# Kernel tuning notes

Hardware: AMD Instinct MI355X
Metric: run time of the kernel (lower is better)

## Reference

```python
import jax, jax.numpy as jnp
from jax import lax
import numpy as np

B_, C_, H_, W_ = 4, 512, 128, 128   # batch, channels, height, width
HEADS, K, PAD = 8, 3, 1


def setup_inputs() -> dict:
    key = jax.random.key(0)
    ks = jax.random.split(key, 12)
    s = 0.1
    return {
        "output": jax.random.normal(ks[0], (B_, C_, H_, W_), jnp.float32),
        "attn": jax.random.uniform(ks[1], (B_ * W_, HEADS, H_, H_), dtype=jnp.float32),
        "Wv": jax.random.normal(ks[2], (C_, C_), jnp.float32) * 0.02,   # value_conv 1x1
        "bv": jnp.zeros((C_,), jnp.float32),
        "W1": jax.random.normal(ks[3], (K, HEADS, 1, K), jnp.float32) * s,  # conv1 (1,k)
        "b1": jax.random.normal(ks[4], (K,), jnp.float32) * s,
        "W2": jax.random.normal(ks[5], (K, 1, 3, 3), jnp.float32) * s,      # depthwise 3x3
        "b2": jax.random.normal(ks[6], (K,), jnp.float32) * s,
        "Wl": jax.random.normal(ks[7], (K, 1), jnp.float32) * s,            # Linear(1,k)
        "bl": jax.random.normal(ks[8], (K,), jnp.float32) * s,
        "Wo": jax.random.normal(ks[9], (C_, C_), jnp.float32) * 0.02,   # out_conv 1x1
        "bo": jnp.zeros((C_,), jnp.float32),
    }


def _forward(output, attn, Wv, bv, W1, b1, W2, b2, Wl, bl, Wo, bo):
    b, c, h, w = output.shape
    B, heads, p, _ = attn.shape        # B = b*w, p = h (attn_type='height')
    d = c // heads
    k = W1.shape[0]

    # value_conv: 1x1 conv == channel GEMM
    value = jnp.einsum('bchw,oc->bohw', output, Wv) + bv[None, :, None, None]
    # [b,c,h,w] -> [b*w, heads, h, d]
    v = value.transpose(0, 3, 2, 1).reshape(B, p, heads, d).transpose(0, 2, 1, 3)

    # --- Adaptive_kernel: per-position kernel A[b,i,j,m] and per-head gate V[b,n,m] ---
    a = lax.conv_general_dilated(attn, W1, (1, 1), ((0, 0), (PAD, PAD)))
    a = jax.nn.relu(a + b1[None, :, None, None])
    a = lax.conv_general_dilated(a, W2, (1, 1), ((1, 1), (1, 1)), feature_group_count=k)
    a = jax.nn.relu(a + b2[None, :, None, None])
    A = a.transpose(0, 2, 3, 1)                      # [B,p,p,k]
    vm = v.mean(axis=(2, 3))                         # AdaptiveAvgPool2d(1): [B,heads]
    V = vm[..., None] * Wl[:, 0] + bl                # Linear(1,k): [B,heads,k]

    # --- adaptive_conv: involution along width with zero padding ---
    ap = jnp.pad(attn, ((0, 0), (0, 0), (0, 0), (PAD, PAD)))
    attn_new = jnp.zeros_like(attn)
    for m in range(k):  # fixed small kernel width; avoids [B,n,p,p,k] materialization
        attn_new = attn_new + ap[..., m:m + p] * A[:, None, :, :, m] * V[:, :, None, None, m]

    # attn @ value and fold back to [b,c,h,w]
    out = jnp.einsum('bnij,bnjd->bnid', attn_new, v)
    out = out.reshape(b, w, heads, h, d).transpose(0, 2, 4, 3, 1).reshape(b, c, h, w)
    out = jnp.einsum('bchw,oc->bohw', out, Wo) + bo[None, :, None, None]
    return out, attn_new


def reference(output, attn, Wv, bv, W1, b1, W2, b2, Wl, bl, Wo, bo):
    return _forward(output, attn, Wv, bv, W1, b1, W2, b2, Wl, bl, Wo, bo)
```

## Files before the change

kernel.cpp:

```cpp
#include <hip/hip_runtime.h>
#include <hip/hip_bf16.h>

#define BATCH 4
#define C 512
#define H 128
#define W 128
#define HW (H*W)
#define CHW (C*HW)
#define NH 8
#define D 64
#define P 128
#define BB (BATCH*W)
#define OUT0_SIZE ((size_t)BATCH*C*H*W)

__global__ __launch_bounds__(256) void k_gemm_value(
    const float* __restrict__ X, const float* __restrict__ Wv,
    const float* __restrict__ bv, float* __restrict__ out)
{
    const int row = blockIdx.x;
    const int b = row >> 7, h = row & 127;
    const int o0 = blockIdx.y * 128;
    const float* xbase = X + (size_t)b*CHW + (size_t)h*W;
    __shared__ float sA[16][132];
    __shared__ float sB[16][132];
    const int tid = threadIdx.x;
    const int tx = tid & 15, ty = tid >> 4;
    float acc[8][8] = {};
    for (int c0 = 0; c0 < C; c0 += 16) {
        #pragma unroll
        for (int it = 0; it < 8; it++) {
            int f = tid + it*256;
            int m = f >> 4, cc = f & 15;
            sA[cc][m] = Wv[(size_t)(o0+m)*C + c0 + cc];
        }
        #pragma unroll
        for (int it = 0; it < 8; it++) {
            int f = tid + it*256;
            int cc = f >> 7, w = f & 127;
            sB[cc][w] = xbase[(size_t)(c0+cc)*HW + w];
        }
        __syncthreads();
        #pragma unroll
        for (int cc = 0; cc < 16; cc++) {
            float a[8], br[8];
            #pragma unroll
            for (int m = 0; m < 8; m++) a[m] = sA[cc][ty*8+m];
            #pragma unroll
            for (int n = 0; n < 8; n++) br[n] = sB[cc][tx*8+n];
            #pragma unroll
            for (int m = 0; m < 8; m++)
                #pragma unroll
                for (int n = 0; n < 8; n++) acc[m][n] += a[m]*br[n];
        }
        __syncthreads();
    }
    #pragma unroll
    for (int m = 0; m < 8; m++) {
        int o = o0 + ty*8 + m;
        float bias = bv[o];
        float* dst = out + (size_t)b*CHW + (size_t)o*HW + (size_t)h*W + tx*8;
        #pragma unroll
        for (int n = 0; n < 8; n++) dst[n] = acc[m][n] + bias;
    }
}

__global__ __launch_bounds__(256) void k_transpose_v(
    const float* __restrict__ val, float* __restrict__ v)
{
    int g = blockIdx.x;
    int i = g & 127, n = (g >> 7) & 7, b = g >> 10;
    __shared__ float s[64][129];
    int tid = threadIdx.x;
    const float* src = val + (size_t)b*CHW + (size_t)(n*64)*HW + (size_t)i*W;
    #pragma unroll
    for (int it = 0; it < 32; it++) {
        int f = tid + it*256;
        int dd = f >> 7, w = f & 127;
        s[dd][w] = src[(size_t)dd*HW + w];
    }
    __syncthreads();
    float* dst = v + (size_t)n*8192 + (size_t)i*64;
    #pragma unroll
    for (int it = 0; it < 32; it++) {
        int f = tid + it*256;
        int w = f >> 6, dd = f & 63;
        dst[(size_t)(b*W + w)*65536 + dd] = s[dd][w];
    }
}

__global__ __launch_bounds__(256) void k_vm(
    const float* __restrict__ v, float* __restrict__ vm)
{
    int g = blockIdx.x;
    const float4* src = (const float4*)(v + (size_t)g*8192);
    int tid = threadIdx.x;
    float sum = 0.f;
    #pragma unroll
    for (int it = 0; it < 8; it++) {
        float4 x = src[tid + it*256];
        sum += x.x + x.y + x.z + x.w;
    }
    #pragma unroll
    for (int off = 32; off; off >>= 1) sum += __shfl_down(sum, off, 64);
    __shared__ float partial[4];
    if ((tid & 63) == 0) partial[tid >> 6] = sum;
    __syncthreads();
    if (tid == 0) vm[g] = (partial[0]+partial[1]+partial[2]+partial[3]) * (1.0f/8192.0f);
}

__global__ __launch_bounds__(256) void k_conv(
    const float* __restrict__ attn, const float* __restrict__ W1,
    const float* __restrict__ b1, const float* __restrict__ W2,
    const float* __restrict__ b2, float* __restrict__ A)
{
    int blk = blockIdx.x;
    int strip = blk & 7, b = blk >> 3;
    int i0 = strip * 16;
    __shared__ float a1s[3][18][128];
    __shared__ float w1s[72], w2s[27], b1s[3], b2s[3];
    int tid = threadIdx.x;
    if (tid < 72) w1s[tid] = W1[tid];
    else if (tid < 99) w2s[tid-72] = W2[tid-72];
    else if (tid < 102) b1s[tid-99] = b1[tid-99];
    else if (tid < 105) b2s[tid-102] = b2[tid-102];
    __syncthreads();
    const float* abase = attn + (size_t)b*NH*HW;
    for (int it = 0; it < 27; it++) {
        int f = tid + it*256;
        int j = f & 127;
        int r = (f >> 7) % 18;
        int kk = f / 2304;
        int i = i0 - 1 + r;
        float vres = 0.f;
        if (i >= 0 && i < P) {
            float s = b1s[kk];
            #pragma unroll
            for (int n = 0; n < 8; n++) {
                const float* ar = abase + (size_t)n*HW + (size_t)i*W;
                float x0 = (j > 0)   ? ar[j-1] : 0.f;
                float x1 = ar[j];
                float x2 = (j < 127) ? ar[j+1] : 0.f;
                s += x0*w1s[kk*24+n*3+0] + x1*w1s[kk*24+n*3+1] + x2*w1s[kk*24+n*3+2];
            }
            vres = fmaxf(s, 0.f);
        }
        a1s[kk][r][j] = vres;
    }
    __syncthreads();
    for (int it = 0; it < 24; it++) {
        int f = tid + it*256;
        int j = f & 127;
        int lr = (f >> 7) & 15;
        int kk = f >> 11;
        float s = b2s[kk];
        #pragma unroll
        for (int u = 0; u < 3; u++) {
            #pragma unroll
            for (int t = 0; t < 3; t++) {
                int jj = j + t - 1;
                float x = (jj >= 0 && jj < 128) ? a1s[kk][lr+u][jj] : 0.f;
                s += x * w2s[kk*9+u*3+t];
            }
        }
        A[(((size_t)b*3 + kk)*P + (i0+lr))*P + j] = fmaxf(s, 0.f);
    }
}

__global__ __launch_bounds__(256) void k_attn_new(
    const float* __restrict__ attn, const float* __restrict__ A,
    const float* __restrict__ vm, const float* __restrict__ Wl,
    const float* __restrict__ bl, float* __restrict__ anew)
{
    int blk = blockIdx.x;
    int i = blk & 127, bw = blk >> 7;
    __shared__ float As[3][128];
    __shared__ float rows[8][130];
    __shared__ float Vs[8][3];
    int tid = threadIdx.x;
    for (int f = tid; f < 384; f += 256) {
        int m = f >> 7, j = f & 127;
        As[m][j] = A[(((size_t)bw*3 + m)*P + i)*P + j];
    }
    if (tid < 24) {
        int n = tid / 3, m = tid % 3;
        Vs[n][m] = vm[bw*8 + n] * Wl[m] + bl[m];
    }
    const float* ab = attn + (size_t)bw*NH*HW + (size_t)i*W;
    #pragma unroll
    for (int f0 = 0; f0 < 1024; f0 += 256) {
        int f = tid + f0;
        int n = f >> 7, j = f & 127;
        rows[n][j+1] = ab[(size_t)n*HW + j];
    }
    if (tid < 8) { rows[tid][0] = 0.f; rows[tid][129] = 0.f; }
    __syncthreads();
    int n = tid >> 5, jj = tid & 31;
    float v0 = Vs[n][0], v1 = Vs[n][1], v2 = Vs[n][2];
    float* dst = anew + ((size_t)bw*NH + n)*HW + (size_t)i*W;
    #pragma unroll
    for (int q = 0; q < 4; q++) {
        int j = jj + q*32;
        float r = rows[n][j]*As[0][j]*v0 + rows[n][j+1]*As[1][j]*v1 + rows[n][j+2]*As[2][j]*v2;
        dst[j] = r;
    }
}

__global__ __launch_bounds__(256) void k_gemm_av(
    const float* __restrict__ anew, const float* __restrict__ v,
    float* __restrict__ op)
{
    int g = blockIdx.x;
    const float* Abase = anew + (size_t)g*HW;
    const float* Bbase = v + (size_t)g*8192;
    float* obase = op + (size_t)g*8192;
    __shared__ float sAT[16][132];
    __shared__ float sB[16][68];
    int tid = threadIdx.x;
    int tx = tid & 15, ty = tid >> 4;
    float acc[8][4] = {};
    for (int j0 = 0; j0 < 128; j0 += 16) {
        #pragma unroll
        for (int it = 0; it < 8; it++) {
            int f = tid + it*256;
            int i = f >> 4, jc = f & 15;
            sAT[jc][i] = Abase[(size_t)i*128 + j0 + jc];
        }
        #pragma unroll
        for (int it = 0; it < 4; it++) {
            int f = tid + it*256;
            int jc = f >> 6, dd = f & 63;
            sB[jc][dd] = Bbase[(size_t)(j0+jc)*64 + dd];
        }
        __syncthreads();
        #pragma unroll
        for (int jc = 0; jc < 16; jc++) {
            float a[8], br[4];
            #pragma unroll
            for (int m = 0; m < 8; m++) a[m] = sAT[jc][ty*8+m];
            #pragma unroll
            for (int n2 = 0; n2 < 4; n2++) br[n2] = sB[jc][tx*4+n2];
            #pragma unroll
            for (int m = 0; m < 8; m++)
                #pragma unroll
                for (int n2 = 0; n2 < 4; n2++) acc[m][n2] += a[m]*br[n2];
        }
        __syncthreads();
    }
    #pragma unroll
    for (int m = 0; m < 8; m++) {
        float* dst = obase + (size_t)(ty*8+m)*64 + tx*4;
        dst[0]=acc[m][0]; dst[1]=acc[m][1]; dst[2]=acc[m][2]; dst[3]=acc[m][3];
    }
}

__global__ __launch_bounds__(256) void k_gemm_out(
    const float* __restrict__ op, const float* __restrict__ Wo,
    const float* __restrict__ bo, float* __restrict__ out)
{
    int row = blockIdx.x;
    int b = row >> 7, i = row & 127;
    int o0 = blockIdx.y * 128;
    __shared__ float sW[32][132];
    __shared__ float sX[32][132];
    int tid = threadIdx.x;
    int tx = tid & 15, ty = tid >> 4;
    float acc[8][8] = {};
    const float* opbase = op + (size_t)(b*W)*65536 + (size_t)i*64;
    for (int chunk = 0; chunk < 16; chunk++) {
        int c0 = chunk*32;
        int n = c0 >> 6, ddb = c0 & 63;
        #pragma unroll
        for (int it = 0; it < 16; it++) {
            int f = tid + it*256;
            int m = f >> 5, cc = f & 31;
            sW[cc][m] = Wo[(size_t)(o0+m)*C + c0 + cc];
        }
        #pragma unroll
        for (int it = 0; it < 16; it++) {
            int f = tid + it*256;
            int w = f >> 5, cc = f & 31;
            sX[cc][w] = opbase[(size_t)w*65536 + (size_t)n*8192 + ddb + cc];
        }
        __syncthreads();
        #pragma unroll
        for (int cc = 0; cc < 32; cc++) {
            float a[8], br[8];
            #pragma unroll
            for (int m = 0; m < 8; m++) a[m] = sW[cc][ty*8+m];
            #pragma unroll
            for (int nn = 0; nn < 8; nn++) br[nn] = sX[cc][tx*8+nn];
            #pragma unroll
            for (int m = 0; m < 8; m++)
                #pragma unroll
                for (int nn = 0; nn < 8; nn++) acc[m][nn] += a[m]*br[nn];
        }
        __syncthreads();
    }
    #pragma unroll
    for (int m = 0; m < 8; m++) {
        int o = o0 + ty*8 + m;
        float bias = bo[o];
        float* dst = out + (size_t)b*CHW + (size_t)o*HW + (size_t)i*W + tx*8;
        #pragma unroll
        for (int n = 0; n < 8; n++) dst[n] = acc[m][n] + bias;
    }
}

extern "C" void kernel_launch(void* const* d_in, const int* in_sizes, int n_in,
                              void* d_out, int out_size, void* d_ws, size_t ws_size,
                              hipStream_t stream)
{
    const float* X    = (const float*)d_in[0];
    const float* attn = (const float*)d_in[1];
    const float* Wv   = (const float*)d_in[2];
    const float* bv   = (const float*)d_in[3];
    const float* W1   = (const float*)d_in[4];
    const float* b1   = (const float*)d_in[5];
    const float* W2   = (const float*)d_in[6];
    const float* b2   = (const float*)d_in[7];
    const float* Wl   = (const float*)d_in[8];
    const float* bl   = (const float*)d_in[9];
    const float* Wo   = (const float*)d_in[10];
    const float* bo   = (const float*)d_in[11];

    float* out  = (float*)d_out;
    float* anew = (float*)d_out + OUT0_SIZE;

    float* A = out;

    float* ws = (float*)d_ws;
    float* value   = ws;
    float* v       = ws + 33554432;
    float* vm      = ws + 67108864;
    float* out_pre = value;

    k_gemm_value<<<dim3(BATCH*H, C/128), 256, 0, stream>>>(X, Wv, bv, value);
    k_transpose_v<<<BATCH*NH*P, 256, 0, stream>>>(value, v);
    k_vm<<<BB*NH, 256, 0, stream>>>(v, vm);
    k_conv<<<BB*(P/16), 256, 0, stream>>>(attn, W1, b1, W2, b2, A);
    k_attn_new<<<BB*P, 256, 0, stream>>>(attn, A, vm, Wl, bl, anew);
    k_gemm_av<<<BB*NH, 256, 0, stream>>>(anew, v, out_pre);
    k_gemm_out<<<dim3(BATCH*P, C/128), 256, 0, stream>>>(out_pre, Wo, bo, out);
}
```

Before: 1.967 ms.

## Use split-bf16 MFMA for value and output 1x1 conv GEMMs

Replaces the two FP32 SIMT channel GEMMs with MFMA bf16 kernels that emulate fp32 through hi/lo bf16 splitting (three MFMAs per tile). Input X is transposed into channel-contiguous hi/lo buffers, and the value GEMM now writes directly into the per-head v layout, which removes the separate transpose kernel. The attention GEMM emits hi/lo bf16 outputs for the final GEMM. The aim is to move the dominant GEMM FLOPs onto matrix cores, at the cost of extra conversion passes, operands loaded straight from global memory without LDS staging, and slightly reduced precision.

```diff
diff --git a/kernel.cpp b/kernel.cpp
--- a/kernel.cpp
+++ b/kernel.cpp
@@ -1,5 +1,9 @@
 #include <hip/hip_runtime.h>
 #include <hip/hip_bf16.h>
+
+typedef __attribute__((ext_vector_type(8))) short bf16x8;
+typedef __attribute__((ext_vector_type(4))) float f32x4;
+typedef __attribute__((ext_vector_type(4))) unsigned short u16x4;
 
 #define BATCH 4
 #define C 512
@@ -13,78 +17,112 @@
 #define BB (BATCH*W)
 #define OUT0_SIZE ((size_t)BATCH*C*H*W)
 
-__global__ __launch_bounds__(256) void k_gemm_value(
-    const float* __restrict__ X, const float* __restrict__ Wv,
-    const float* __restrict__ bv, float* __restrict__ out)
-{
-    const int row = blockIdx.x;
-    const int b = row >> 7, h = row & 127;
-    const int o0 = blockIdx.y * 128;
-    const float* xbase = X + (size_t)b*CHW + (size_t)h*W;
-    __shared__ float sA[16][132];
-    __shared__ float sB[16][132];
-    const int tid = threadIdx.x;
-    const int tx = tid & 15, ty = tid >> 4;
-    float acc[8][8] = {};
-    for (int c0 = 0; c0 < C; c0 += 16) {
-        #pragma unroll
-        for (int it = 0; it < 8; it++) {
-            int f = tid + it*256;
-            int m = f >> 4, cc = f & 15;
-            sA[cc][m] = Wv[(size_t)(o0+m)*C + c0 + cc];
-        }
-        #pragma unroll
-        for (int it = 0; it < 8; it++) {
-            int f = tid + it*256;
-            int cc = f >> 7, w = f & 127;
-            sB[cc][w] = xbase[(size_t)(c0+cc)*HW + w];
-        }
-        __syncthreads();
-        #pragma unroll
-        for (int cc = 0; cc < 16; cc++) {
-            float a[8], br[8];
-            #pragma unroll
-            for (int m = 0; m < 8; m++) a[m] = sA[cc][ty*8+m];
-            #pragma unroll
-            for (int n = 0; n < 8; n++) br[n] = sB[cc][tx*8+n];
-            #pragma unroll
-            for (int m = 0; m < 8; m++)
-                #pragma unroll
-                for (int n = 0; n < 8; n++) acc[m][n] += a[m]*br[n];
-        }
-        __syncthreads();
-    }
-    #pragma unroll
-    for (int m = 0; m < 8; m++) {
-        int o = o0 + ty*8 + m;
-        float bias = bv[o];
-        float* dst = out + (size_t)b*CHW + (size_t)o*HW + (size_t)h*W + tx*8;
-        #pragma unroll
-        for (int n = 0; n < 8; n++) dst[n] = acc[m][n] + bias;
-    }
-}
-
-__global__ __launch_bounds__(256) void k_transpose_v(
-    const float* __restrict__ val, float* __restrict__ v)
-{
-    int g = blockIdx.x;
-    int i = g & 127, n = (g >> 7) & 7, b = g >> 10;
+__device__ __forceinline__ unsigned short f2bf(float x) {
+    unsigned u = __float_as_uint(x);
+    unsigned r = u + 0x7fffu + ((u >> 16) & 1u);
+    return (unsigned short)(r >> 16);
+}
+__device__ __forceinline__ float bf2f(unsigned short b) {
+    return __uint_as_float(((unsigned)b) << 16);
+}
+
+__global__ __launch_bounds__(256) void k_cvt_w(
+    const float* __restrict__ src, unsigned short* __restrict__ hi,
+    unsigned short* __restrict__ lo, int n)
+{
+    int idx = blockIdx.x * 256 + threadIdx.x;
+    if (idx < n) {
+        float x = src[idx];
+        unsigned short h = f2bf(x);
+        unsigned short l = f2bf(x - bf2f(h));
+        hi[idx] = h; lo[idx] = l;
+    }
+}
+
+__global__ __launch_bounds__(256) void k_xt(
+    const float* __restrict__ X, unsigned short* __restrict__ Xh,
+    unsigned short* __restrict__ Xl)
+{
+    int blk = blockIdx.x;
+    int cblk = blk & 7, i = (blk >> 3) & 127, b = blk >> 10;
+    int c0 = cblk * 64;
     __shared__ float s[64][129];
     int tid = threadIdx.x;
-    const float* src = val + (size_t)b*CHW + (size_t)(n*64)*HW + (size_t)i*W;
+    const float* src = X + (size_t)b*CHW + (size_t)c0*HW + (size_t)i*W;
     #pragma unroll
     for (int it = 0; it < 32; it++) {
         int f = tid + it*256;
-        int dd = f >> 7, w = f & 127;
-        s[dd][w] = src[(size_t)dd*HW + w];
+        int w = f & 127, cc = f >> 7;
+        s[cc][w] = src[(size_t)cc*HW + w];
     }
     __syncthreads();
-    float* dst = v + (size_t)n*8192 + (size_t)i*64;
+    size_t dbase = ((size_t)(b*128 + i)*128)*512 + c0;
     #pragma unroll
     for (int it = 0; it < 32; it++) {
         int f = tid + it*256;
-        int w = f >> 6, dd = f & 63;
-        dst[(size_t)(b*W + w)*65536 + dd] = s[dd][w];
+        int cc = f & 63, w = f >> 6;
+        float x = s[cc][w];
+        unsigned short h = f2bf(x);
+        unsigned short l = f2bf(x - bf2f(h));
+        size_t idx = dbase + (size_t)w*512 + cc;
+        Xh[idx] = h; Xl[idx] = l;
+    }
+}
+
+__global__ __launch_bounds__(256) void k_gemm_value_mfma(
+    const unsigned short* __restrict__ Xh, const unsigned short* __restrict__ Xl,
+    const unsigned short* __restrict__ Wh, const unsigned short* __restrict__ Wl,
+    const float* __restrict__ bv, float* __restrict__ v)
+{
+    const int bi = blockIdx.x;
+    const int b = bi >> 7, i = bi & 127;
+    const int o0 = blockIdx.y * 128;
+    const int tid = threadIdx.x;
+    const int wave = tid >> 6, lane = tid & 63;
+    const int sl = lane & 15, g = lane >> 4;
+    const int w0 = wave * 32;
+
+    const unsigned short* a0h = Xh + ((size_t)bi*128 + w0 + sl)*512 + g*8;
+    const unsigned short* a0l = Xl + ((size_t)bi*128 + w0 + sl)*512 + g*8;
+    const unsigned short* bh  = Wh + (size_t)(o0 + sl)*512 + g*8;
+    const unsigned short* bl  = Wl + (size_t)(o0 + sl)*512 + g*8;
+
+    f32x4 acc[2][8];
+    #pragma unroll
+    for (int ms = 0; ms < 2; ms++)
+        #pragma unroll
+        for (int ns = 0; ns < 8; ns++) acc[ms][ns] = (f32x4){0.f,0.f,0.f,0.f};
+
+    for (int c0 = 0; c0 < 512; c0 += 32) {
+        bf16x8 Ah0 = *(const bf16x8*)(a0h + c0);
+        bf16x8 Al0 = *(const bf16x8*)(a0l + c0);
+        bf16x8 Ah1 = *(const bf16x8*)(a0h + 16*512 + c0);
+        bf16x8 Al1 = *(const bf16x8*)(a0l + 16*512 + c0);
+        #pragma unroll
+        for (int ns = 0; ns < 8; ns++) {
+            bf16x8 Bh = *(const bf16x8*)(bh + (size_t)ns*16*512 + c0);
+            bf16x8 Bl = *(const bf16x8*)(bl + (size_t)ns*16*512 + c0);
+            acc[0][ns] = __builtin_amdgcn_mfma_f32_16x16x32_bf16(Ah0, Bh, acc[0][ns], 0,0,0);
+            acc[0][ns] = __builtin_amdgcn_mfma_f32_16x16x32_bf16(Al0, Bh, acc[0][ns], 0,0,0);
+            acc[0][ns] = __builtin_amdgcn_mfma_f32_16x16x32_bf16(Ah0, Bl, acc[0][ns], 0,0,0);
+            acc[1][ns] = __builtin_amdgcn_mfma_f32_16x16x32_bf16(Ah1, Bh, acc[1][ns], 0,0,0);
+            acc[1][ns] = __builtin_amdgcn_mfma_f32_16x16x32_bf16(Al1, Bh, acc[1][ns], 0,0,0);
+            acc[1][ns] = __builtin_amdgcn_mfma_f32_16x16x32_bf16(Ah1, Bl, acc[1][ns], 0,0,0);
+        }
+    }
+    #pragma unroll
+    for (int ns = 0; ns < 8; ns++) {
+        int o = o0 + ns*16 + sl;
+        float bias = bv[o];
+        size_t vb = (size_t)(b*128)*65536 + (size_t)(o >> 6)*8192 + (size_t)i*64 + (o & 63);
+        #pragma unroll
+        for (int ms = 0; ms < 2; ms++) {
+            #pragma unroll
+            for (int r = 0; r < 4; r++) {
+                int w = w0 + ms*16 + g*4 + r;
+                v[vb + (size_t)w*65536] = acc[ms][ns][r] + bias;
+            }
+        }
     }
 }
 
@@ -207,12 +245,11 @@
 
 __global__ __launch_bounds__(256) void k_gemm_av(
     const float* __restrict__ anew, const float* __restrict__ v,
-    float* __restrict__ op)
+    unsigned short* __restrict__ oph, unsigned short* __restrict__ opl)
 {
     int g = blockIdx.x;
     const float* Abase = anew + (size_t)g*HW;
     const float* Bbase = v + (size_t)g*8192;
-    float* obase = op + (size_t)g*8192;
     __shared__ float sAT[16][132];
     __shared__ float sB[16][68];
     int tid = threadIdx.x;
@@ -248,61 +285,83 @@
     }
     #pragma unroll
     for (int m = 0; m < 8; m++) {
-        float* dst = obase + (size_t)(ty*8+m)*64 + tx*4;
-        dst[0]=acc[m][0]; dst[1]=acc[m][1]; dst[2]=acc[m][2]; dst[3]=acc[m][3];
-    }
-}
-
-__global__ __launch_bounds__(256) void k_gemm_out(
-    const float* __restrict__ op, const float* __restrict__ Wo,
-    const float* __restrict__ bo, float* __restrict__ out)
-{
-    int row = blockIdx.x;
-    int b = row >> 7, i = row & 127;
-    int o0 = blockIdx.y * 128;
-    __shared__ float sW[32][132];
-    __shared__ float sX[32][132];
-    int tid = threadIdx.x;
-    int tx = tid & 15, ty = tid >> 4;
-    float acc[8][8] = {};
-    const float* opbase = op + (size_t)(b*W)*65536 + (size_t)i*64;
-    for (int chunk = 0; chunk < 16; chunk++) {
-        int c0 = chunk*32;
-        int n = c0 >> 6, ddb = c0 & 63;
-        #pragma unroll
-        for (int it = 0; it < 16; it++) {
-            int f = tid + it*256;
-            int m = f >> 5, cc = f & 31;
-            sW[cc][m] = Wo[(size_t)(o0+m)*C + c0 + cc];
-        }
-        #pragma unroll
-        for (int it = 0; it < 16; it++) {
-            int f = tid + it*256;
-            int w = f >> 5, cc = f & 31;
-            sX[cc][w] = opbase[(size_t)w*65536 + (size_t)n*8192 + ddb + cc];
-        }
-        __syncthreads();
-        #pragma unroll
-        for (int cc = 0; cc < 32; cc++) {
-            float a[8], br[8];
-            #pragma unroll
-            for (int m = 0; m < 8; m++) a[m] = sW[cc][ty*8+m];
-            #pragma unroll
-            for (int nn = 0; nn < 8; nn++) br[nn] = sX[cc][tx*8+nn];
-            #pragma unroll
-            for (int m = 0; m < 8; m++)
-                #pragma unroll
-                for (int nn = 0; nn < 8; nn++) acc[m][nn] += a[m]*br[nn];
-        }
-        __syncthreads();
-    }
-    #pragma unroll
-    for (int m = 0; m < 8; m++) {
-        int o = o0 + ty*8 + m;
-        float bias = bo[o];
-        float* dst = out + (size_t)b*CHW + (size_t)o*HW + (size_t)i*W + tx*8;
-        #pragma unroll
-        for (int n = 0; n < 8; n++) dst[n] = acc[m][n] + bias;
+        size_t base = (size_t)g*8192 + (size_t)(ty*8+m)*64 + tx*4;
+        u16x4 hv, lv;
+        #pragma unroll
+        for (int n2 = 0; n2 < 4; n2++) {
+            float x = acc[m][n2];
+            unsigned short h = f2bf(x);
+            unsigned short l = f2bf(x - bf2f(h));
+            hv[n2] = h; lv[n2] = l;
+        }
+        *(u16x4*)(oph + base) = hv;
+        *(u16x4*)(opl + base) = lv;
+    }
+}
+
+__global__ __launch_bounds__(256) void k_gemm_out_mfma(
+    const unsigned short* __restrict__ Ph, const unsigned short* __restrict__ Pl,
+    const float* __restrict__ Wo, const float* __restrict__ bo,
+    float* __restrict__ out)
+{
+    const int bi = blockIdx.x;
+    const int b = bi >> 7, i = bi & 127;
+    const int tid = threadIdx.x;
+    const int wave = tid >> 6, lane = tid & 63;
+    const int sl = lane & 15, g = lane >> 4;
+    const int ow = blockIdx.y * 128 + wave * 32;
+
+    const float* wo0 = Wo + (size_t)(ow + sl)*512 + g*8;
+    const size_t pb = (size_t)(b*128 + sl)*65536 + (size_t)i*64;
+
+    f32x4 acc[2][8];
+    #pragma unroll
+    for (int ms = 0; ms < 2; ms++)
+        #pragma unroll
+        for (int ns = 0; ns < 8; ns++) acc[ms][ns] = (f32x4){0.f,0.f,0.f,0.f};
+
+    for (int c0 = 0; c0 < 512; c0 += 32) {
+        int cA = c0 + g*8;
+        bf16x8 Ah0, Al0, Ah1, Al1;
+        #pragma unroll
+        for (int e = 0; e < 8; e++) {
+            float x = wo0[c0 + e];
+            unsigned short h = f2bf(x);
+            Ah0[e] = (short)h; Al0[e] = (short)f2bf(x - bf2f(h));
+        }
+        #pragma unroll
+        for (int e = 0; e < 8; e++) {
+            float x = wo0[16*512 + c0 + e];
+            unsigned short h = f2bf(x);
+            Ah1[e] = (short)h; Al1[e] = (short)f2bf(x - bf2f(h));
+        }
+        size_t coff = (size_t)(cA >> 6)*8192 + (cA & 63);
+        #pragma unroll
+        for (int ns = 0; ns < 8; ns++) {
+            const unsigned short* bp = Ph + pb + (size_t)ns*16*65536 + coff;
+            const unsigned short* bq = Pl + pb + (size_t)ns*16*65536 + coff;
+            bf16x8 Bh = *(const bf16x8*)bp;
+            bf16x8 Bl = *(const bf16x8*)bq;
+            acc[0][ns] = __builtin_amdgcn_mfma_f32_16x16x32_bf16(Ah0, Bh, acc[0][ns], 0,0,0);
+            acc[0][ns] = __builtin_amdgcn_mfma_f32_16x16x32_bf16(Al0, Bh, acc[0][ns], 0,0,0);
+            acc[0][ns] = __builtin_amdgcn_mfma_f32_16x16x32_bf16(Ah0, Bl, acc[0][ns], 0,0,0);
+            acc[1][ns] = __builtin_amdgcn_mfma_f32_16x16x32_bf16(Ah1, Bh, acc[1][ns], 0,0,0);
+            acc[1][ns] = __builtin_amdgcn_mfma_f32_16x16x32_bf16(Al1, Bh, acc[1][ns], 0,0,0);
+            acc[1][ns] = __builtin_amdgcn_mfma_f32_16x16x32_bf16(Ah1, Bl, acc[1][ns], 0,0,0);
+        }
+    }
+    #pragma unroll
+    for (int ms = 0; ms < 2; ms++) {
+        #pragma unroll
+        for (int r = 0; r < 4; r++) {
+            int o = ow + ms*16 + g*4 + r;
+            float bias = bo[o];
+            float* dst = out + (size_t)b*CHW + (size_t)o*HW + (size_t)i*W;
+            #pragma unroll
+            for (int ns = 0; ns < 8; ns++) {
+                dst[ns*16 + sl] = acc[ms][ns][r] + bias;
+            }
+        }
     }
 }
 
@@ -327,18 +386,23 @@
     float* anew = (float*)d_out + OUT0_SIZE;
 
     float* A = out;
+    unsigned short* wvh = (unsigned short*)(out + 25165824);
+    unsigned short* wvl = (unsigned short*)(out + 25296896);
+    float* vm = out + 25427968;
 
     float* ws = (float*)d_ws;
-    float* value   = ws;
-    float* v       = ws + 33554432;
-    float* vm      = ws + 67108864;
-    float* out_pre = value;
-
-    k_gemm_value<<<dim3(BATCH*H, C/128), 256, 0, stream>>>(X, Wv, bv, value);
-    k_transpose_v<<<BATCH*NH*P, 256, 0, stream>>>(value, v);
+    float* v = ws;
+    unsigned short* xth = (unsigned short*)(ws + 33554432);
+    unsigned short* xtl = (unsigned short*)(ws + 50331648);
+    unsigned short* oph = xth;
+    unsigned short* opl = xtl;
+
+    k_cvt_w<<<1024, 256, 0, stream>>>(Wv, wvh, wvl, 262144);
+    k_xt<<<4096, 256, 0, stream>>>(X, xth, xtl);
+    k_gemm_value_mfma<<<dim3(512, 4), 256, 0, stream>>>(xth, xtl, wvh, wvl, bv, v);
     k_vm<<<BB*NH, 256, 0, stream>>>(v, vm);
     k_conv<<<BB*(P/16), 256, 0, stream>>>(attn, W1, b1, W2, b2, A);
     k_attn_new<<<BB*P, 256, 0, stream>>>(attn, A, vm, Wl, bl, anew);
-    k_gemm_av<<<BB*NH, 256, 0, stream>>>(anew, v, out_pre);
-    k_gemm_out<<<dim3(BATCH*P, C/128), 256, 0, stream>>>(out_pre, Wo, bo, out);
-}
+    k_gemm_av<<<BB*NH, 256, 0, stream>>>(anew, v, oph, opl);
+    k_gemm_out_mfma<<<dim3(512, 4), 256, 0, stream>>>(oph, opl, Wo, bo, out);
+}
```

Measured after the change: 1.589 ms. 19.2% less time.
